# Optimization experiments

Hardware: AMD Instinct MI355X
Metric: run time of the kernel (lower is better)

The kernel has to match this reference:

```python
import jax, jax.numpy as jnp
import numpy as np

N_NODES = 50000
N_EDGES = 800000
IN_DIM = 128
HID = 32
HEADS = 4
OUT_DIM = 64
NEG_SLOPE = 0.2  # DGL GATConv default


def setup_inputs() -> dict:
    key = jax.random.key(0)
    ks = jax.random.split(key, 20)

    def glorot(k, shape):
        fan = shape[0] + shape[-1]
        return (jax.random.normal(k, shape, jnp.float32) * np.sqrt(2.0 / fan)).astype(jnp.float32)

    inp = {
        "h": jax.random.normal(ks[0], (N_NODES, IN_DIM), jnp.float32),
        "src": jax.random.randint(ks[1], (N_EDGES,), 0, N_NODES, jnp.int32),
        "dst": jax.random.randint(ks[2], (N_EDGES,), 0, N_NODES, jnp.int32),
        # layer 0: in_dim -> hidden, HEADS heads, relu
        "W1": glorot(ks[3], (IN_DIM, HEADS * HID)),
        "al1": glorot(ks[4], (HEADS, HID)),
        "ar1": glorot(ks[5], (HEADS, HID)),
        "b1": jnp.zeros((HEADS * HID,), jnp.float32),
        # layer 1 (hidden): hidden*heads -> hidden, HEADS heads, relu
        "W2": glorot(ks[6], (HEADS * HID, HEADS * HID)),
        "al2": glorot(ks[7], (HEADS, HID)),
        "ar2": glorot(ks[8], (HEADS, HID)),
        "b2": jnp.zeros((HEADS * HID,), jnp.float32),
        # layer 2 (output): hidden*heads -> out_dim, 1 head, no activation
        "W3": glorot(ks[9], (HEADS * HID, OUT_DIM)),
        "al3": glorot(ks[10], (1, OUT_DIM)),
        "ar3": glorot(ks[11], (1, OUT_DIM)),
        "b3": jnp.zeros((OUT_DIM,), jnp.float32),
    }
    return inp


def gat_conv(h, src, dst, W, attn_l, attn_r, bias, heads, out_dim, use_relu):
    n = h.shape[0]
    feat = (h @ W).reshape(n, heads, out_dim)              # [N,H,D]
    el = jnp.sum(feat * attn_l[None], axis=-1)             # [N,H]
    er = jnp.sum(feat * attn_r[None], axis=-1)             # [N,H]
    e = jax.nn.leaky_relu(el[src] + er[dst], NEG_SLOPE)    # [E,H] per-edge logits
    # segment softmax over incoming edges of each dst node
    emax = jax.ops.segment_max(e, dst, num_segments=n)     # [N,H] (-inf for isolated nodes, never gathered)
    ee = jnp.exp(e - emax[dst])                            # [E,H]
    denom = jax.ops.segment_sum(ee, dst, num_segments=n)   # [N,H]
    alpha = ee / denom[dst]                                # [E,H]
    msg = feat[src] * alpha[:, :, None]                    # [E,H,D] gather + weight
    out = jax.ops.segment_sum(msg, dst, num_segments=n)    # [N,H,D] scatter-add
    out = out + bias.reshape(1, heads, out_dim)
    if use_relu:
        out = jax.nn.relu(out)
    return out.reshape(n, heads * out_dim)


def reference(h, src, dst, W1, al1, ar1, b1, W2, al2, ar2, b2, W3, al3, ar3, b3):
    # dropout is identity in eval mode
    h1 = gat_conv(h, src, dst, W1, al1, ar1, b1, HEADS, HID, True)
    h2 = gat_conv(h1, src, dst, W2, al2, ar2, b2, HEADS, HID, True)
    h3 = gat_conv(h2, src, dst, W3, al3, ar3, b3, 1, OUT_DIM, False)
    return h3
```

## Files before the change

kernel.cpp:

```cpp
#include <hip/hip_runtime.h>
#include <hip/hip_fp16.h>

#define NNODES 50000
#define NEDGES 800000
#define HISTB 256

__device__ __forceinline__ float leaky(float x) { return x >= 0.f ? x : 0.2f * x; }

typedef _Float16 f16x8 __attribute__((ext_vector_type(8)));
typedef float f32x4 __attribute__((ext_vector_type(4)));

struct __align__(8)  half4v { __half2 h0, h1; };
struct __align__(16) half8v { __half2 h0, h1, h2, h3; };

__global__ __launch_bounds__(256) void init_k(const float* __restrict__ W1,
                                              const float* __restrict__ W2,
                                              const float* __restrict__ W3,
                                              __half* __restrict__ Wt,
                                              int* __restrict__ cnt) {
    int i = blockIdx.x * 256 + threadIdx.x;
    if (i < NNODES) cnt[i] = 0;
    if (i < 16384) {
        int k = i >> 7, c = i & 127;
        Wt[c * 128 + k] = __float2half_rn(W1[i]);
    } else if (i < 32768) {
        int e = i - 16384, k = e >> 7, c = e & 127;
        Wt[16384 + c * 128 + k] = __float2half_rn(W2[e]);
    } else if (i < 40960) {
        int e = i - 32768, k = e >> 6, c = e & 63;
        Wt[32768 + c * 128 + k] = __float2half_rn(W3[e]);
    }
}

template<int F, int H, bool FP16IN, bool DO_HIST, int CSPLIT>
__global__ __launch_bounds__(256) void gemm_mfma_k(const void* __restrict__ Xv,
                                                   const __half* __restrict__ Wt,
                                                   const float* __restrict__ al,
                                                   const float* __restrict__ ar,
                                                   __half* __restrict__ Yh,
                                                   float* __restrict__ el,
                                                   float* __restrict__ er, int n,
                                                   int nGemm,
                                                   const int* __restrict__ dst,
                                                   int* __restrict__ cnt,
                                                   int* __restrict__ rank) {
    constexpr int K = 128;
    constexpr int ROWS = 64 / CSPLIT;
    constexpr int NTW = F / 16 / CSPLIT;
    constexpr int LDC = F + 8;

    if (DO_HIST && blockIdx.x >= nGemm) {
        int b = blockIdx.x - nGemm;
        for (int e = b * 256 + threadIdx.x; e < NEDGES; e += HISTB * 256)
            rank[e] = atomicAdd(&cnt[dst[e]], 1);
        return;
    }

    __shared__ __align__(16) __half Cs[ROWS * LDC];

    const int tid = threadIdx.x;
    const int wv = tid >> 6, lane = tid & 63;
    const int rs = wv / CSPLIT;
    const int ch = wv % CSPLIT;
    const int cl = lane & 15, kg = lane >> 4;
    const int r0 = blockIdx.x * ROWS;
    const int rowA = r0 + 16 * rs + cl;
    const int rA = rowA < n ? rowA : n - 1;

    f32x4 acc[NTW];
    #pragma unroll
    for (int t = 0; t < NTW; t++) acc[t] = (f32x4){0.f, 0.f, 0.f, 0.f};

    #pragma unroll
    for (int ks = 0; ks < K / 32; ks++) {
        f16x8 a;
        if constexpr (FP16IN) {
            a = *(const f16x8*)((const __half*)Xv + (size_t)rA * K + ks * 32 + kg * 8);
        } else {
            const float* Xp = (const float*)Xv + (size_t)rA * K + ks * 32 + kg * 8;
            float4 x0 = *(const float4*)Xp;
            float4 x1 = *(const float4*)(Xp + 4);
            a[0] = (_Float16)x0.x; a[1] = (_Float16)x0.y;
            a[2] = (_Float16)x0.z; a[3] = (_Float16)x0.w;
            a[4] = (_Float16)x1.x; a[5] = (_Float16)x1.y;
            a[6] = (_Float16)x1.z; a[7] = (_Float16)x1.w;
        }
        #pragma unroll
        for (int t = 0; t < NTW; t++) {
            int tg = ch * NTW + t;
            f16x8 b = *(const f16x8*)(Wt + (size_t)(16 * tg + cl) * K + ks * 32 + kg * 8);
            acc[t] = __builtin_amdgcn_mfma_f32_16x16x32_f16(a, b, acc[t], 0, 0, 0);
        }
    }

    #pragma unroll
    for (int t = 0; t < NTW; t++)
        #pragma unroll
        for (int j = 0; j < 4; j++)
            Cs[(16 * rs + 4 * kg + j) * LDC + (ch * NTW + t) * 16 + cl] =
                __float2half_rn(acc[t][j]);
    __syncthreads();
    {
        constexpr int SEGS = F / 8;
        #pragma unroll
        for (int s = 0; s < ROWS * SEGS / 256; s++) {
            int idx = s * 256 + tid;
            int row = idx / SEGS, seg = idx % SEGS;
            int grow = r0 + row;
            if (grow < n)
                *(half8v*)&Yh[(size_t)grow * F + seg * 8] =
                    *(const half8v*)&Cs[row * LDC + seg * 8];
        }
    }

    float alv[NTW], arv[NTW];
    #pragma unroll
    for (int t = 0; t < NTW; t++) {
        alv[t] = al[(ch * NTW + t) * 16 + cl];
        arv[t] = ar[(ch * NTW + t) * 16 + cl];
    }

    if (H == 1) {
        float pl[4], pr[4];
        #pragma unroll
        for (int j = 0; j < 4; j++) {
            pl[j] = 0.f; pr[j] = 0.f;
            #pragma unroll
            for (int t = 0; t < NTW; t++) { pl[j] += acc[t][j] * alv[t]; pr[j] += acc[t][j] * arv[t]; }
        }
        #pragma unroll
        for (int off = 1; off < 16; off <<= 1)
            #pragma unroll
            for (int j = 0; j < 4; j++) { pl[j] += __shfl_xor(pl[j], off); pr[j] += __shfl_xor(pr[j], off); }
        if (cl == 0)
            #pragma unroll
            for (int j = 0; j < 4; j++) {
                int row = r0 + 16 * rs + 4 * kg + j;
                if (row < n) { el[row] = pl[j]; er[row] = pr[j]; }
            }
    } else {
        constexpr int HPW = NTW / 2;
        float pl[HPW][4], pr[HPW][4];
        #pragma unroll
        for (int hh = 0; hh < HPW; hh++)
            #pragma unroll
            for (int j = 0; j < 4; j++) {
                pl[hh][j] = acc[2 * hh][j] * alv[2 * hh] + acc[2 * hh + 1][j] * alv[2 * hh + 1];
                pr[hh][j] = acc[2 * hh][j] * arv[2 * hh] + acc[2 * hh + 1][j] * arv[2 * hh + 1];
            }
        #pragma unroll
        for (int off = 1; off < 16; off <<= 1)
            #pragma unroll
            for (int hh = 0; hh < HPW; hh++)
                #pragma unroll
                for (int j = 0; j < 4; j++) {
                    pl[hh][j] += __shfl_xor(pl[hh][j], off);
                    pr[hh][j] += __shfl_xor(pr[hh][j], off);
                }
        if (cl == 0)
            #pragma unroll
            for (int j = 0; j < 4; j++) {
                int row = r0 + 16 * rs + 4 * kg + j;
                if (row < n)
                    #pragma unroll
                    for (int hh = 0; hh < HPW; hh++) {
                        el[row * H + ch * HPW + hh] = pl[hh][j];
                        er[row * H + ch * HPW + hh] = pr[hh][j];
                    }
            }
    }
}

__global__ void scan_blk_k(const int* __restrict__ cnt, int* __restrict__ offs,
                           int* __restrict__ bsum, int n) {
    __shared__ int sm[256];
    int tid = threadIdx.x;
    int i = blockIdx.x * 256 + tid;
    int v = (i < n) ? cnt[i] : 0;
    sm[tid] = v;
    __syncthreads();
    for (int off = 1; off < 256; off <<= 1) {
        int t = (tid >= off) ? sm[tid - off] : 0;
        __syncthreads();
        sm[tid] += t;
        __syncthreads();
    }
    if (i < n) offs[i] = sm[tid] - v;
    if (tid == 255) bsum[blockIdx.x] = sm[255];
}

__global__ void scan_addtop_k(int* __restrict__ offs, const int* __restrict__ bsum,
                              int n, int nb) {
    __shared__ int sm[256];
    int tid = threadIdx.x;
    int v = (tid < nb) ? bsum[tid] : 0;
    sm[tid] = v;
    __syncthreads();
    for (int off = 1; off < 256; off <<= 1) {
        int t = (tid >= off) ? sm[tid - off] : 0;
        __syncthreads();
        sm[tid] += t;
        __syncthreads();
    }
    int prefix = (blockIdx.x > 0) ? sm[blockIdx.x - 1] : 0;
    int i = blockIdx.x * 256 + tid;
    if (i < n) offs[i] += prefix;
    if (i == 0) offs[n] = NEDGES;
}

__global__ void scatter_k(const int* __restrict__ src, const int* __restrict__ dst,
                          const int* __restrict__ rank, const int* __restrict__ offs,
                          int* __restrict__ esrc) {
    int e = blockIdx.x * blockDim.x + threadIdx.x;
    if (e < NEDGES) esrc[offs[dst[e]] + rank[e]] = src[e];
}

__global__ __launch_bounds__(256) void node_agg4_k(const int* __restrict__ offs,
                                                   const int* __restrict__ esrc,
                                                   const float* __restrict__ el,
                                                   const float* __restrict__ er,
                                                   const __half* __restrict__ feat,
                                                   const float* __restrict__ bias,
                                                   __half* __restrict__ out) {
    const int lane = threadIdx.x & 63;
    const int gw0 = (blockIdx.x * 256 + threadIdx.x) >> 6;
    const int NW = (gridDim.x * 256) >> 6;

    const int h  = lane & 3;
    const int q  = lane >> 4;
    const int cl = lane & 15;
    const int hd = cl >> 2;

    float4 ba = *(const float4*)&bias[8 * cl];
    float4 bb = *(const float4*)&bias[8 * cl + 4];

    for (int wid = gw0; wid < NNODES; wid += NW) {
        int beg = offs[wid], end = offs[wid + 1];
        float erh = er[wid * 4 + h];

        float acc[8] = {0.f, 0.f, 0.f, 0.f, 0.f, 0.f, 0.f, 0.f};
        float dsum = 0.f;
        for (int base = beg; base < end; base += 16) {
            int rem = end - base;
            if (rem > 16) rem = 16;
            int sv = 0;
            if (lane < rem) sv = esrc[base + lane];
            int se = __shfl(sv, lane >> 2);
            float p = 0.f;
            if ((lane >> 2) < rem)
                p = __expf(leaky(el[se * 4 + h] + erh));
            dsum += p;
            #pragma unroll
            for (int e = 0; e < 16 && e < rem; e += 4) {
                int eidx = e + q;
                int s = __shfl(sv, eidx);
                float a = __shfl(p, eidx * 4 + hd);
                half8v hv = *(const half8v*)&feat[(size_t)s * 128 + 8 * cl];
                float2 f0 = __half22float2(hv.h0);
                float2 f1 = __half22float2(hv.h1);
                float2 f2 = __half22float2(hv.h2);
                float2 f3 = __half22float2(hv.h3);
                acc[0] += f0.x * a; acc[1] += f0.y * a;
                acc[2] += f1.x * a; acc[3] += f1.y * a;
                acc[4] += f2.x * a; acc[5] += f2.y * a;
                acc[6] += f3.x * a; acc[7] += f3.y * a;
            }
        }
        #pragma unroll
        for (int c = 0; c < 8; c++) {
            acc[c] += __shfl_xor(acc[c], 16);
            acc[c] += __shfl_xor(acc[c], 32);
        }
        #pragma unroll
        for (int off = 4; off < 64; off <<= 1) dsum += __shfl_xor(dsum, off);
        float dh = __shfl(dsum, hd);
        float inv = dh > 0.f ? 1.f / dh : 0.f;
        if (q == 0) {
            float v0 = fmaxf(acc[0] * inv + ba.x, 0.f), v1 = fmaxf(acc[1] * inv + ba.y, 0.f);
            float v2 = fmaxf(acc[2] * inv + ba.z, 0.f), v3 = fmaxf(acc[3] * inv + ba.w, 0.f);
            float v4 = fmaxf(acc[4] * inv + bb.x, 0.f), v5 = fmaxf(acc[5] * inv + bb.y, 0.f);
            float v6 = fmaxf(acc[6] * inv + bb.z, 0.f), v7 = fmaxf(acc[7] * inv + bb.w, 0.f);
            half8v hv;
            hv.h0 = __halves2half2(__float2half_rn(v0), __float2half_rn(v1));
            hv.h1 = __halves2half2(__float2half_rn(v2), __float2half_rn(v3));
            hv.h2 = __halves2half2(__float2half_rn(v4), __float2half_rn(v5));
            hv.h3 = __halves2half2(__float2half_rn(v6), __float2half_rn(v7));
            *(half8v*)&out[(size_t)wid * 128 + 8 * cl] = hv;
        }
    }
}

__global__ __launch_bounds__(256) void node_agg1_k(const int* __restrict__ offs,
                                                   const int* __restrict__ esrc,
                                                   const float* __restrict__ el,
                                                   const float* __restrict__ er,
                                                   const __half* __restrict__ feat,
                                                   const float* __restrict__ bias,
                                                   float* __restrict__ out) {
    const int lane = threadIdx.x & 63;
    const int gw0 = (blockIdx.x * 256 + threadIdx.x) >> 6;
    const int NW = (gridDim.x * 256) >> 6;

    const int q  = lane >> 4;
    const int cl = lane & 15;
    float4 b4 = *(const float4*)&bias[4 * cl];

    for (int wid = gw0; wid < NNODES; wid += NW) {
        int beg = offs[wid], end = offs[wid + 1];
        float erd = er[wid];

        float acc[4] = {0.f, 0.f, 0.f, 0.f};
        float dsum = 0.f;
        for (int base = beg; base < end; base += 64) {
            int rem = end - base;
            if (rem > 64) rem = 64;
            int sv = 0;
            float p = 0.f;
            if (lane < rem) {
                sv = esrc[base + lane];
                p = __expf(leaky(el[sv] + erd));
            }
            dsum += p;
            #pragma unroll 4
            for (int e = 0; e < rem; e += 4) {
                int eidx = e + q;
                int s = __shfl(sv, eidx);
                float a = __shfl(p, eidx);
                half4v hv = *(const half4v*)&feat[(size_t)s * 64 + 4 * cl];
                float2 f0 = __half22float2(hv.h0);
                float2 f1 = __half22float2(hv.h1);
                acc[0] += f0.x * a; acc[1] += f0.y * a;
                acc[2] += f1.x * a; acc[3] += f1.y * a;
            }
        }
        #pragma unroll
        for (int c = 0; c < 4; c++) {
            acc[c] += __shfl_xor(acc[c], 16);
            acc[c] += __shfl_xor(acc[c], 32);
        }
        #pragma unroll
        for (int off = 1; off < 64; off <<= 1) dsum += __shfl_xor(dsum, off);
        float inv = dsum > 0.f ? 1.f / dsum : 0.f;
        if (q == 0) {
            *(float4*)&out[(size_t)wid * 64 + 4 * cl] =
                make_float4(acc[0] * inv + b4.x, acc[1] * inv + b4.y,
                            acc[2] * inv + b4.z, acc[3] * inv + b4.w);
        }
    }
}

extern "C" void kernel_launch(void* const* d_in, const int* in_sizes, int n_in,
                              void* d_out, int out_size, void* d_ws, size_t ws_size,
                              hipStream_t stream) {
    const float* h   = (const float*)d_in[0];
    const int*   src = (const int*)d_in[1];
    const int*   dst = (const int*)d_in[2];
    const float* W1  = (const float*)d_in[3];
    const float* al1 = (const float*)d_in[4];
    const float* ar1 = (const float*)d_in[5];
    const float* b1  = (const float*)d_in[6];
    const float* W2  = (const float*)d_in[7];
    const float* al2 = (const float*)d_in[8];
    const float* ar2 = (const float*)d_in[9];
    const float* b2  = (const float*)d_in[10];
    const float* W3  = (const float*)d_in[11];
    const float* al3 = (const float*)d_in[12];
    const float* ar3 = (const float*)d_in[13];
    const float* b3  = (const float*)d_in[14];
    float* out = (float*)d_out;

    const int n = NNODES;
    __half* feat16 = (__half*)d_ws;
    __half* hbuf16 = feat16 + (size_t)n * 128;
    float*  el     = (float*)(hbuf16 + (size_t)n * 128);
    float*  er     = el + (size_t)n * 4;
    int*    cnt    = (int*)(er + (size_t)n * 4);
    int*    offs   = cnt + n;
    int*    esrc   = offs + (n + 1);
    int*    bsum   = esrc + NEDGES;
    int*    rank   = bsum + 256;
    __half* wt     = (__half*)(rank + NEDGES);
    __half* wt1 = wt, *wt2 = wt + 16384, *wt3 = wt + 32768;

    const int gemm32 = (n + 31) / 32;
    const int gemm64 = (n + 63) / 64;
    const int nBlk = (n + 255) / 256;
    const int eBlk = (NEDGES + 255) / 256;
    const int aggBlk = 2048;

    init_k<<<nBlk, 256, 0, stream>>>(W1, W2, W3, wt, cnt);

    gemm_mfma_k<128, 4, false, true, 2><<<gemm32 + HISTB, 256, 0, stream>>>(
        h, wt1, al1, ar1, feat16, el, er, n, gemm32, dst, cnt, rank);

    scan_blk_k<<<nBlk, 256, 0, stream>>>(cnt, offs, bsum, n);
    scan_addtop_k<<<nBlk, 256, 0, stream>>>(offs, bsum, n, nBlk);
    scatter_k<<<eBlk, 256, 0, stream>>>(src, dst, rank, offs, esrc);

    node_agg4_k<<<aggBlk, 256, 0, stream>>>(offs, esrc, el, er, feat16, b1, hbuf16);

    gemm_mfma_k<128, 4, true, false, 2><<<gemm32, 256, 0, stream>>>(
        hbuf16, wt2, al2, ar2, feat16, el, er, n, gemm32, nullptr, nullptr, nullptr);
    node_agg4_k<<<aggBlk, 256, 0, stream>>>(offs, esrc, el, er, feat16, b2, hbuf16);

    gemm_mfma_k<64, 1, true, false, 1><<<gemm64, 256, 0, stream>>>(
        hbuf16, wt3, al3, ar3, feat16, el, er, n, gemm64, nullptr, nullptr, nullptr);
    node_agg1_k<<<aggBlk, 256, 0, stream>>>(offs, esrc, el, er, feat16, b3, out);
}
```

Measured before the change: 217.2 us.

## Fuse node aggregation with next layer's MFMA GEMM and attention projections

Replaces each node_agg4 kernel plus the following GEMM with one kernel. It aggregates 64 destination rows into shared memory, then runs the MFMA GEMM on that tile and writes the next layer's features along with el/er. This removes the round trip of the hidden activations through global memory and two kernel launches. The cost is a 512-thread block per 64-row tile with serial per-wave row aggregation, which lowers parallelism for the gather phase compared with the grid-stride aggregation kernel. Buffers are split into A/B/C so that reads and writes within a fused kernel do not alias.

```diff
diff --git a/kernel.cpp b/kernel.cpp
--- a/kernel.cpp
+++ b/kernel.cpp
@@ -120,27 +120,16 @@
         arv[t] = ar[(ch * NTW + t) * 16 + cl];
     }
 
+    constexpr int HPW = (H == 1) ? 1 : NTW / 2;
+    float pl[HPW][4], pr[HPW][4];
     if (H == 1) {
-        float pl[4], pr[4];
         #pragma unroll
         for (int j = 0; j < 4; j++) {
-            pl[j] = 0.f; pr[j] = 0.f;
-            #pragma unroll
-            for (int t = 0; t < NTW; t++) { pl[j] += acc[t][j] * alv[t]; pr[j] += acc[t][j] * arv[t]; }
-        }
-        #pragma unroll
-        for (int off = 1; off < 16; off <<= 1)
-            #pragma unroll
-            for (int j = 0; j < 4; j++) { pl[j] += __shfl_xor(pl[j], off); pr[j] += __shfl_xor(pr[j], off); }
-        if (cl == 0)
-            #pragma unroll
-            for (int j = 0; j < 4; j++) {
-                int row = r0 + 16 * rs + 4 * kg + j;
-                if (row < n) { el[row] = pl[j]; er[row] = pr[j]; }
-            }
+            pl[0][j] = 0.f; pr[0][j] = 0.f;
+            #pragma unroll
+            for (int t = 0; t < NTW; t++) { pl[0][j] += acc[t][j] * alv[t]; pr[0][j] += acc[t][j] * arv[t]; }
+        }
     } else {
-        constexpr int HPW = NTW / 2;
-        float pl[HPW][4], pr[HPW][4];
         #pragma unroll
         for (int hh = 0; hh < HPW; hh++)
             #pragma unroll
@@ -148,6 +137,194 @@
                 pl[hh][j] = acc[2 * hh][j] * alv[2 * hh] + acc[2 * hh + 1][j] * alv[2 * hh + 1];
                 pr[hh][j] = acc[2 * hh][j] * arv[2 * hh] + acc[2 * hh + 1][j] * arv[2 * hh + 1];
             }
+    }
+    #pragma unroll
+    for (int off = 1; off < 16; off <<= 1)
+        #pragma unroll
+        for (int hh = 0; hh < HPW; hh++)
+            #pragma unroll
+            for (int j = 0; j < 4; j++) {
+                pl[hh][j] += __shfl_xor(pl[hh][j], off);
+                pr[hh][j] += __shfl_xor(pr[hh][j], off);
+            }
+    if (cl == 0)
+        #pragma unroll
+        for (int j = 0; j < 4; j++) {
+            int row = r0 + 16 * rs + 4 * kg + j;
+            if (row < n) {
+                if (H == 1) { el[row] = pl[0][j]; er[row] = pr[0][j]; }
+                else
+                    #pragma unroll
+                    for (int hh = 0; hh < HPW; hh++) {
+                        el[row * H + ch * HPW + hh] = pl[hh][j];
+                        er[row * H + ch * HPW + hh] = pr[hh][j];
+                    }
+            }
+        }
+}
+
+template<int F, int H>
+__global__ __launch_bounds__(512) void fused_agg_gemm_k(
+        const int* __restrict__ offs, const int* __restrict__ esrc,
+        const float* __restrict__ el, const float* __restrict__ er,
+        const __half* __restrict__ feat, const float* __restrict__ bias,
+        const __half* __restrict__ Wt,
+        const float* __restrict__ al, const float* __restrict__ ar,
+        __half* __restrict__ Yh, float* __restrict__ elo,
+        float* __restrict__ ero, int n) {
+    constexpr int K = 128;
+    constexpr int LDK = K + 8;
+    constexpr int CS = (F == 128) ? 2 : 1;
+    constexpr int NTW = F / 16 / CS;
+    __shared__ __align__(16) __half Ls[64 * LDK];
+
+    const int tid = threadIdx.x;
+    const int wv = tid >> 6;
+    const int lane = tid & 63;
+    const int r0 = blockIdx.x * 64;
+
+    {
+        const int h  = lane & 3;
+        const int q  = lane >> 4;
+        const int cl = lane & 15;
+        const int hd = cl >> 2;
+        float4 ba = *(const float4*)&bias[8 * cl];
+        float4 bb = *(const float4*)&bias[8 * cl + 4];
+
+        for (int i = 0; i < 8; i++) {
+            int row = wv * 8 + i;
+            int wid = r0 + row;
+            if (wid >= n) {
+                if (q == 0) {
+                    __half2 z = __float2half2_rn(0.f);
+                    half8v hv; hv.h0 = z; hv.h1 = z; hv.h2 = z; hv.h3 = z;
+                    *(half8v*)&Ls[row * LDK + 8 * cl] = hv;
+                }
+                continue;
+            }
+            int beg = offs[wid], end = offs[wid + 1];
+            float erh = er[wid * 4 + h];
+
+            float acc[8] = {0.f, 0.f, 0.f, 0.f, 0.f, 0.f, 0.f, 0.f};
+            float dsum = 0.f;
+            for (int base = beg; base < end; base += 16) {
+                int rem = end - base;
+                if (rem > 16) rem = 16;
+                int sv = 0;
+                if (lane < rem) sv = esrc[base + lane];
+                int se = __shfl(sv, lane >> 2);
+                float p = 0.f;
+                if ((lane >> 2) < rem)
+                    p = __expf(leaky(el[se * 4 + h] + erh));
+                dsum += p;
+                #pragma unroll
+                for (int e = 0; e < 16 && e < rem; e += 4) {
+                    int eidx = e + q;
+                    int s = __shfl(sv, eidx);
+                    float a = __shfl(p, eidx * 4 + hd);
+                    half8v hv = *(const half8v*)&feat[(size_t)s * 128 + 8 * cl];
+                    float2 f0 = __half22float2(hv.h0);
+                    float2 f1 = __half22float2(hv.h1);
+                    float2 f2 = __half22float2(hv.h2);
+                    float2 f3 = __half22float2(hv.h3);
+                    acc[0] += f0.x * a; acc[1] += f0.y * a;
+                    acc[2] += f1.x * a; acc[3] += f1.y * a;
+                    acc[4] += f2.x * a; acc[5] += f2.y * a;
+                    acc[6] += f3.x * a; acc[7] += f3.y * a;
+                }
+            }
+            #pragma unroll
+            for (int c = 0; c < 8; c++) {
+                acc[c] += __shfl_xor(acc[c], 16);
+                acc[c] += __shfl_xor(acc[c], 32);
+            }
+            #pragma unroll
+            for (int off = 4; off < 64; off <<= 1) dsum += __shfl_xor(dsum, off);
+            float dh = __shfl(dsum, hd);
+            float inv = dh > 0.f ? 1.f / dh : 0.f;
+            if (q == 0) {
+                float v0 = fmaxf(acc[0] * inv + ba.x, 0.f), v1 = fmaxf(acc[1] * inv + ba.y, 0.f);
+                float v2 = fmaxf(acc[2] * inv + ba.z, 0.f), v3 = fmaxf(acc[3] * inv + ba.w, 0.f);
+                float v4 = fmaxf(acc[4] * inv + bb.x, 0.f), v5 = fmaxf(acc[5] * inv + bb.y, 0.f);
+                float v6 = fmaxf(acc[6] * inv + bb.z, 0.f), v7 = fmaxf(acc[7] * inv + bb.w, 0.f);
+                half8v hv;
+                hv.h0 = __halves2half2(__float2half_rn(v0), __float2half_rn(v1));
+                hv.h1 = __halves2half2(__float2half_rn(v2), __float2half_rn(v3));
+                hv.h2 = __halves2half2(__float2half_rn(v4), __float2half_rn(v5));
+                hv.h3 = __halves2half2(__float2half_rn(v6), __float2half_rn(v7));
+                *(half8v*)&Ls[row * LDK + 8 * cl] = hv;
+            }
+        }
+    }
+    __syncthreads();
+
+    const int cl = lane & 15, kg = lane >> 4;
+    const bool active = wv < 4 * CS;
+    const int rs = (CS == 2) ? (wv >> 1) : wv;
+    const int ch = (CS == 2) ? (wv & 1) : 0;
+
+    f32x4 acc2[NTW];
+    #pragma unroll
+    for (int t = 0; t < NTW; t++) acc2[t] = (f32x4){0.f, 0.f, 0.f, 0.f};
+
+    if (active) {
+        #pragma unroll
+        for (int ks = 0; ks < K / 32; ks++) {
+            f16x8 a = *(const f16x8*)&Ls[(16 * rs + cl) * LDK + ks * 32 + kg * 8];
+            #pragma unroll
+            for (int t = 0; t < NTW; t++) {
+                int tg = ch * NTW + t;
+                f16x8 b = *(const f16x8*)(Wt + (size_t)(16 * tg + cl) * K + ks * 32 + kg * 8);
+                acc2[t] = __builtin_amdgcn_mfma_f32_16x16x32_f16(a, b, acc2[t], 0, 0, 0);
+            }
+        }
+    }
+    __syncthreads();
+    if (active) {
+        #pragma unroll
+        for (int t = 0; t < NTW; t++)
+            #pragma unroll
+            for (int j = 0; j < 4; j++)
+                Ls[(16 * rs + 4 * kg + j) * LDK + (ch * NTW + t) * 16 + cl] =
+                    __float2half_rn(acc2[t][j]);
+    }
+    __syncthreads();
+    {
+        constexpr int SEGS = F / 8;
+        for (int idx = tid; idx < 64 * SEGS; idx += 512) {
+            int row = idx / SEGS, seg = idx % SEGS;
+            int grow = r0 + row;
+            if (grow < n)
+                *(half8v*)&Yh[(size_t)grow * F + seg * 8] =
+                    *(const half8v*)&Ls[row * LDK + seg * 8];
+        }
+    }
+
+    if (active) {
+        float alv[NTW], arv[NTW];
+        #pragma unroll
+        for (int t = 0; t < NTW; t++) {
+            alv[t] = al[(ch * NTW + t) * 16 + cl];
+            arv[t] = ar[(ch * NTW + t) * 16 + cl];
+        }
+        constexpr int HPW = (H == 1) ? 1 : NTW / 2;
+        float pl[HPW][4], pr[HPW][4];
+        if (H == 1) {
+            #pragma unroll
+            for (int j = 0; j < 4; j++) {
+                pl[0][j] = 0.f; pr[0][j] = 0.f;
+                #pragma unroll
+                for (int t = 0; t < NTW; t++) { pl[0][j] += acc2[t][j] * alv[t]; pr[0][j] += acc2[t][j] * arv[t]; }
+            }
+        } else {
+            #pragma unroll
+            for (int hh = 0; hh < HPW; hh++)
+                #pragma unroll
+                for (int j = 0; j < 4; j++) {
+                    pl[hh][j] = acc2[2 * hh][j] * alv[2 * hh] + acc2[2 * hh + 1][j] * alv[2 * hh + 1];
+                    pr[hh][j] = acc2[2 * hh][j] * arv[2 * hh] + acc2[2 * hh + 1][j] * arv[2 * hh + 1];
+                }
+        }
         #pragma unroll
         for (int off = 1; off < 16; off <<= 1)
             #pragma unroll
@@ -161,12 +338,15 @@
             #pragma unroll
             for (int j = 0; j < 4; j++) {
                 int row = r0 + 16 * rs + 4 * kg + j;
-                if (row < n)
-                    #pragma unroll
-                    for (int hh = 0; hh < HPW; hh++) {
-                        el[row * H + ch * HPW + hh] = pl[hh][j];
-                        er[row * H + ch * HPW + hh] = pr[hh][j];
-                    }
+                if (row < n) {
+                    if (H == 1) { elo[row] = pl[0][j]; ero[row] = pr[0][j]; }
+                    else
+                        #pragma unroll
+                        for (int hh = 0; hh < HPW; hh++) {
+                            elo[row * H + ch * HPW + hh] = pl[hh][j];
+                            ero[row * H + ch * HPW + hh] = pr[hh][j];
+                        }
+                }
             }
     }
 }
@@ -213,81 +393,6 @@
                           int* __restrict__ esrc) {
     int e = blockIdx.x * blockDim.x + threadIdx.x;
     if (e < NEDGES) esrc[offs[dst[e]] + rank[e]] = src[e];
-}
-
-__global__ __launch_bounds__(256) void node_agg4_k(const int* __restrict__ offs,
-                                                   const int* __restrict__ esrc,
-                                                   const float* __restrict__ el,
-                                                   const float* __restrict__ er,
-                                                   const __half* __restrict__ feat,
-                                                   const float* __restrict__ bias,
-                                                   __half* __restrict__ out) {
-    const int lane = threadIdx.x & 63;
-    const int gw0 = (blockIdx.x * 256 + threadIdx.x) >> 6;
-    const int NW = (gridDim.x * 256) >> 6;
-
-    const int h  = lane & 3;
-    const int q  = lane >> 4;
-    const int cl = lane & 15;
-    const int hd = cl >> 2;
-
-    float4 ba = *(const float4*)&bias[8 * cl];
-    float4 bb = *(const float4*)&bias[8 * cl + 4];
-
-    for (int wid = gw0; wid < NNODES; wid += NW) {
-        int beg = offs[wid], end = offs[wid + 1];
-        float erh = er[wid * 4 + h];
-
-        float acc[8] = {0.f, 0.f, 0.f, 0.f, 0.f, 0.f, 0.f, 0.f};
-        float dsum = 0.f;
-        for (int base = beg; base < end; base += 16) {
-            int rem = end - base;
-            if (rem > 16) rem = 16;
-            int sv = 0;
-            if (lane < rem) sv = esrc[base + lane];
-            int se = __shfl(sv, lane >> 2);
-            float p = 0.f;
-            if ((lane >> 2) < rem)
-                p = __expf(leaky(el[se * 4 + h] + erh));
-            dsum += p;
-            #pragma unroll
-            for (int e = 0; e < 16 && e < rem; e += 4) {
-                int eidx = e + q;
-                int s = __shfl(sv, eidx);
-                float a = __shfl(p, eidx * 4 + hd);
-                half8v hv = *(const half8v*)&feat[(size_t)s * 128 + 8 * cl];
-                float2 f0 = __half22float2(hv.h0);
-                float2 f1 = __half22float2(hv.h1);
-                float2 f2 = __half22float2(hv.h2);
-                float2 f3 = __half22float2(hv.h3);
-                acc[0] += f0.x * a; acc[1] += f0.y * a;
-                acc[2] += f1.x * a; acc[3] += f1.y * a;
-                acc[4] += f2.x * a; acc[5] += f2.y * a;
-                acc[6] += f3.x * a; acc[7] += f3.y * a;
-            }
-        }
-        #pragma unroll
-        for (int c = 0; c < 8; c++) {
-            acc[c] += __shfl_xor(acc[c], 16);
-            acc[c] += __shfl_xor(acc[c], 32);
-        }
-        #pragma unroll
-        for (int off = 4; off < 64; off <<= 1) dsum += __shfl_xor(dsum, off);
-        float dh = __shfl(dsum, hd);
-        float inv = dh > 0.f ? 1.f / dh : 0.f;
-        if (q == 0) {
-            float v0 = fmaxf(acc[0] * inv + ba.x, 0.f), v1 = fmaxf(acc[1] * inv + ba.y, 0.f);
-            float v2 = fmaxf(acc[2] * inv + ba.z, 0.f), v3 = fmaxf(acc[3] * inv + ba.w, 0.f);
-            float v4 = fmaxf(acc[4] * inv + bb.x, 0.f), v5 = fmaxf(acc[5] * inv + bb.y, 0.f);
-            float v6 = fmaxf(acc[6] * inv + bb.z, 0.f), v7 = fmaxf(acc[7] * inv + bb.w, 0.f);
-            half8v hv;
-            hv.h0 = __halves2half2(__float2half_rn(v0), __float2half_rn(v1));
-            hv.h1 = __halves2half2(__float2half_rn(v2), __float2half_rn(v3));
-            hv.h2 = __halves2half2(__float2half_rn(v4), __float2half_rn(v5));
-            hv.h3 = __halves2half2(__float2half_rn(v6), __float2half_rn(v7));
-            *(half8v*)&out[(size_t)wid * 128 + 8 * cl] = hv;
-        }
-    }
 }
 
 __global__ __launch_bounds__(256) void node_agg1_k(const int* __restrict__ offs,
@@ -370,20 +475,25 @@
     float* out = (float*)d_out;
 
     const int n = NNODES;
-    __half* feat16 = (__half*)d_ws;
-    __half* hbuf16 = feat16 + (size_t)n * 128;
-    float*  el     = (float*)(hbuf16 + (size_t)n * 128);
-    float*  er     = el + (size_t)n * 4;
-    int*    cnt    = (int*)(er + (size_t)n * 4);
-    int*    offs   = cnt + n;
-    int*    esrc   = offs + (n + 1);
-    int*    bsum   = esrc + NEDGES;
-    int*    rank   = bsum + 256;
-    __half* wt     = (__half*)(rank + NEDGES);
-    __half* wt1 = wt, *wt2 = wt + 16384, *wt3 = wt + 32768;
+    __half* featA = (__half*)d_ws;
+    __half* featB = featA + (size_t)n * 128;
+    __half* featC = featB + (size_t)n * 128;
+    float*  elA   = (float*)(featC + (size_t)n * 64);
+    float*  erA   = elA + (size_t)n * 4;
+    float*  elB   = erA + (size_t)n * 4;
+    float*  erB   = elB + (size_t)n * 4;
+    float*  elC   = erB + (size_t)n * 4;
+    float*  erC   = elC + n;
+    int*    cnt   = (int*)(erC + n);
+    int*    offs  = cnt + n;
+    int*    esrc  = offs + (n + 1);
+    int*    bsum  = esrc + NEDGES;
+    int*    rank  = bsum + 256;
+    __half* wt    = (__half*)(rank + NEDGES);
+    __half *wt1 = wt, *wt2 = wt + 16384, *wt3 = wt + 32768;
 
     const int gemm32 = (n + 31) / 32;
-    const int gemm64 = (n + 63) / 64;
+    const int tile64 = (n + 63) / 64;
     const int nBlk = (n + 255) / 256;
     const int eBlk = (NEDGES + 255) / 256;
     const int aggBlk = 2048;
@@ -391,19 +501,17 @@
     init_k<<<nBlk, 256, 0, stream>>>(W1, W2, W3, wt, cnt);
 
     gemm_mfma_k<128, 4, false, true, 2><<<gemm32 + HISTB, 256, 0, stream>>>(
-        h, wt1, al1, ar1, feat16, el, er, n, gemm32, dst, cnt, rank);
+        h, wt1, al1, ar1, featA, elA, erA, n, gemm32, dst, cnt, rank);
 
     scan_blk_k<<<nBlk, 256, 0, stream>>>(cnt, offs, bsum, n);
     scan_addtop_k<<<nBlk, 256, 0, stream>>>(offs, bsum, n, nBlk);
     scatter_k<<<eBlk, 256, 0, stream>>>(src, dst, rank, offs, esrc);
 
-    node_agg4_k<<<aggBlk, 256, 0, stream>>>(offs, esrc, el, er, feat16, b1, hbuf16);
-
-    gemm_mfma_k<128, 4, true, false, 2><<<gemm32, 256, 0, stream>>>(
-        hbuf16, wt2, al2, ar2, feat16, el, er, n, gemm32, nullptr, nullptr, nullptr);
-    node_agg4_k<<<aggBlk, 256, 0, stream>>>(offs, esrc, el, er, feat16, b2, hbuf16);
-
-    gemm_mfma_k<64, 1, true, false, 1><<<gemm64, 256, 0, stream>>>(
-        hbuf16, wt3, al3, ar3, feat16, el, er, n, gemm64, nullptr, nullptr, nullptr);
-    node_agg1_k<<<aggBlk, 256, 0, stream>>>(offs, esrc, el, er, feat16, b3, out);
-}
+    fused_agg_gemm_k<128, 4><<<tile64, 512, 0, stream>>>(
+        offs, esrc, elA, erA, featA, b1, wt2, al2, ar2, featB, elB, erB, n);
+
+    fused_agg_gemm_k<64, 1><<<tile64, 512, 0, stream>>>(
+        offs, esrc, elB, erB, featB, b2, wt3, al3, ar3, featC, elC, erC, n);
+
+    node_agg1_k<<<aggBlk, 256, 0, stream>>>(offs, esrc, elC, erC, featC, b3, out);
+}
```

Measured after the change: 258.1 us. 1.19x slower.
